# Optimization experiments

Measured on AMD Instinct MI355X. Metric: run time of the kernel, lower is better.

## Reference

```python
import jax, jax.numpy as jnp
import numpy as np

N_NODES = 100_000
N_EDGES = 1_600_000
IN_DIM = 64
OUT_DIM = 64
EPS = 1e-5


def setup_inputs() -> dict:
    key = jax.random.key(0)
    k1, k2, k3, k4, k5, k6 = jax.random.split(key, 6)
    node = jax.random.normal(k1, (N_NODES, 3), dtype=jnp.float32)
    features = jax.random.normal(k2, (N_NODES, IN_DIM), dtype=jnp.float32)
    # src column covers every node so torch.unique(edges[:,0]) == arange(N_NODES)
    src = (jnp.arange(N_EDGES, dtype=jnp.int64) % N_NODES)
    dst = jax.random.randint(k3, (N_EDGES,), 0, N_NODES, dtype=jnp.int64)
    edges = jnp.stack([src, dst], axis=1)
    # torch.nn.Linear weight: [out_dim, in_dim+3], no bias
    W = jax.random.normal(k4, (OUT_DIM, IN_DIM + 3), dtype=jnp.float32) / np.sqrt(IN_DIM + 3)
    gamma = jnp.ones((OUT_DIM,), dtype=jnp.float32)
    beta = jnp.zeros((OUT_DIM,), dtype=jnp.float32)
    return {"node": node, "features": features, "W": W, "gamma": gamma,
            "beta": beta, "edges": edges}


def reference(node, features, W, gamma, beta, edges):
    src = edges[:, 0]
    dst = edges[:, 1]
    # gather + concat: [E, in_dim + 3]
    msg = jnp.concatenate([features[dst], node[dst] - node[src]], axis=1)
    # linear (no bias): [E, out_dim]
    h = msg @ W.T
    # BatchNorm1d (training mode: biased batch statistics over E rows)
    mean = jnp.mean(h, axis=0)
    var = jnp.mean(jnp.square(h - mean), axis=0)
    h = (h - mean) * jax.lax.rsqrt(var + EPS) * gamma + beta
    h = jax.nn.relu(h)
    # scatter_reduce amax with include_self=True on a zeros tensor:
    # per-destination max, including the initial 0 (relu output >= 0 anyway)
    n = node.shape[0]
    pooled = jnp.zeros((n, h.shape[1]), dtype=features.dtype).at[src].max(h)
    return pooled
```

## Files before the change

kernel.cpp:

```cpp
#include <hip/hip_runtime.h>

#define N_NODES 100000
#define N_EDGES 1600000
#define EPS 1e-5f

typedef __bf16 bf16x8 __attribute__((ext_vector_type(8)));
typedef float  f32x4  __attribute__((ext_vector_type(4)));
typedef unsigned short u16x4 __attribute__((ext_vector_type(4)));

__device__ __forceinline__ unsigned short f2bf(float f) {
  return __builtin_bit_cast(unsigned short, static_cast<__bf16>(f));
}

__global__ __launch_bounds__(256) void prep_kernel(
    const float* __restrict__ feat, const float* __restrict__ W,
    unsigned short* __restrict__ featbf, unsigned short* __restrict__ Wbf) {
  int b = blockIdx.x, t = threadIdx.x;
  if (b < 6250) {
    int idx = (b * 256 + t) * 4;
    f32x4 v = *(const f32x4*)(feat + idx);
    u16x4 o;
    o[0] = f2bf(v[0]); o[1] = f2bf(v[1]); o[2] = f2bf(v[2]); o[3] = f2bf(v[3]);
    *(u16x4*)(featbf + idx) = o;
  } else {
    int wi = (b - 6250) * 256 + t;
    if (wi < 64 * 96) {
      int n = wi / 96, c = wi % 96;
      Wbf[wi] = (c < 67) ? f2bf(W[n * 67 + c]) : (unsigned short)0;
    }
  }
}

__global__ __launch_bounds__(256) void graph_kernel(
    const float* __restrict__ nodep, const int* __restrict__ edges,
    const unsigned short* __restrict__ featbf,
    const unsigned short* __restrict__ Wbf,
    float* __restrict__ maxv, float* __restrict__ minv,
    float* __restrict__ stats, int nwaves) {
  const int lane = threadIdx.x & 63;
  const int wave = (int)((blockIdx.x * blockDim.x + threadIdx.x) >> 6);
  const int c    = lane & 15;
  const int quad = lane >> 4;

  bf16x8 Bfrag[4][3];
#pragma unroll
  for (int t = 0; t < 4; ++t) {
    const unsigned short* wrow = Wbf + (t * 16 + c) * 96 + quad * 8;
#pragma unroll
    for (int s = 0; s < 3; ++s)
      Bfrag[t][s] = *(const bf16x8*)(wrow + s * 32);
  }

  float s1[4] = {0.f, 0.f, 0.f, 0.f};
  float s2[4] = {0.f, 0.f, 0.f, 0.f};

  for (int i = wave; i < N_NODES; i += nwaves) {
    int dst_own = 0;
    if (lane < 16) dst_own = edges[2 * (i + lane * N_NODES) + 1];
    int dst_m = __shfl(dst_own, c, 64);

    const unsigned short* frow = featbf + (size_t)dst_m * 64 + quad * 8;
    bf16x8 A0 = *(const bf16x8*)(frow);
    bf16x8 A1 = *(const bf16x8*)(frow + 32);

    bf16x8 A2;
#pragma unroll
    for (int j = 0; j < 8; ++j) A2[j] = (__bf16)0.0f;
    float nx = nodep[3 * i], ny = nodep[3 * i + 1], nz = nodep[3 * i + 2];
    if (quad == 0) {
      const float* dp = nodep + (size_t)dst_m * 3;
      A2[0] = (__bf16)(dp[0] - nx);
      A2[1] = (__bf16)(dp[1] - ny);
      A2[2] = (__bf16)(dp[2] - nz);
    }

    float mxw = 0.f, mnw = 0.f;
#pragma unroll
    for (int t = 0; t < 4; ++t) {
      f32x4 acc = {0.f, 0.f, 0.f, 0.f};
      acc = __builtin_amdgcn_mfma_f32_16x16x32_bf16(A0, Bfrag[t][0], acc, 0, 0, 0);
      acc = __builtin_amdgcn_mfma_f32_16x16x32_bf16(A1, Bfrag[t][1], acc, 0, 0, 0);
      acc = __builtin_amdgcn_mfma_f32_16x16x32_bf16(A2, Bfrag[t][2], acc, 0, 0, 0);

      float a0 = acc[0], a1 = acc[1], a2 = acc[2], a3 = acc[3];
      s1[t] += (a0 + a1) + (a2 + a3);
      s2[t] += (a0 * a0 + a1 * a1) + (a2 * a2 + a3 * a3);

      float mx = fmaxf(fmaxf(a0, a1), fmaxf(a2, a3));
      float mn = fminf(fminf(a0, a1), fminf(a2, a3));
      mx = fmaxf(mx, __shfl_xor(mx, 16, 64));
      mx = fmaxf(mx, __shfl_xor(mx, 32, 64));
      mn = fminf(mn, __shfl_xor(mn, 16, 64));
      mn = fminf(mn, __shfl_xor(mn, 32, 64));
      if (t == quad) { mxw = mx; mnw = mn; }
    }
    maxv[i * 64 + lane] = mxw;
    minv[i * 64 + lane] = mnw;
  }

#pragma unroll
  for (int t = 0; t < 4; ++t) {
    s1[t] += __shfl_xor(s1[t], 16, 64);
    s1[t] += __shfl_xor(s1[t], 32, 64);
    s2[t] += __shfl_xor(s2[t], 16, 64);
    s2[t] += __shfl_xor(s2[t], 32, 64);
  }
  float s1w = quad == 0 ? s1[0] : quad == 1 ? s1[1] : quad == 2 ? s1[2] : s1[3];
  float s2w = quad == 0 ? s2[0] : quad == 1 ? s2[1] : quad == 2 ? s2[2] : s2[3];
  stats[(size_t)lane * nwaves + wave]        = s1w;
  stats[(size_t)(64 + lane) * nwaves + wave] = s2w;
}

__global__ __launch_bounds__(256) void stats_kernel(
    const float* __restrict__ stats, const float* __restrict__ gamma,
    const float* __restrict__ beta, float* __restrict__ ss, int nwaves) {
  int d = blockIdx.x;
  int t = threadIdx.x;
  const float* r1 = stats + (size_t)d * nwaves;
  const float* r2 = stats + (size_t)(64 + d) * nwaves;
  float a = 0.f, b = 0.f;
  for (int k = t; k < nwaves; k += 256) { a += r1[k]; b += r2[k]; }
  __shared__ float l1[256], l2[256];
  l1[t] = a; l2[t] = b;
  __syncthreads();
  for (int s = 128; s > 0; s >>= 1) {
    if (t < s) { l1[t] += l1[t + s]; l2[t] += l2[t + s]; }
    __syncthreads();
  }
  if (t == 0) {
    const float inv_ne = 1.0f / (float)N_EDGES;
    float mean = l1[0] * inv_ne;
    float var  = fmaxf(l2[0] * inv_ne - mean * mean, 0.f);
    float sc   = gamma[d] * rsqrtf(var + EPS);
    ss[d]      = sc;
    ss[64 + d] = beta[d] - mean * sc;
  }
}

__global__ __launch_bounds__(256) void finalize_kernel(
    const float* __restrict__ minv, const float* __restrict__ ss,
    float* out) {
  int idx = blockIdx.x * 256 + threadIdx.x;
  int d = idx & 63;
  float sc = ss[d], sh = ss[64 + d];
  float v = (sc >= 0.f) ? out[idx] : minv[idx];
  out[idx] = fmaxf(fmaf(v, sc, sh), 0.f);
}

extern "C" void kernel_launch(void* const* d_in, const int* in_sizes, int n_in,
                              void* d_out, int out_size, void* d_ws, size_t ws_size,
                              hipStream_t stream) {
  const float* nodep = (const float*)d_in[0];
  const float* feat  = (const float*)d_in[1];
  const float* W     = (const float*)d_in[2];
  const float* gamma = (const float*)d_in[3];
  const float* beta  = (const float*)d_in[4];
  const int*   edges = (const int*)d_in[5];

  char* ws = (char*)d_ws;
  unsigned short* Wbf    = (unsigned short*)ws;
  unsigned short* featbf = (unsigned short*)(ws + 12288);
  float* minv  = (float*)(ws + 12288 + 12800000);
  float* stats = (float*)(ws + 12288 + 12800000 + 25600000);
  float* ss    = (float*)(ws + 12288 + 12800000 + 25600000 + 4194304);
  float* maxv  = (float*)d_out;

  const int nwaves = 8192;

  prep_kernel<<<6250 + 24, 256, 0, stream>>>(feat, W, featbf, Wbf);
  graph_kernel<<<nwaves / 4, 256, 0, stream>>>(nodep, edges, featbf, Wbf,
                                               maxv, minv, stats, nwaves);
  stats_kernel<<<64, 256, 0, stream>>>(stats, gamma, beta, ss, nwaves);
  finalize_kernel<<<25000, 256, 0, stream>>>(minv, ss, maxv);
}
```

Measured before the change: 174.6 us.

## Software-pipeline gathers in graph kernel with fixed per-wave node schedule

The graph kernel now uses 12500 waves, each handling exactly 8 nodes. All destination indices are preloaded in two registers up front, and the feature and position gathers for the next node are double-buffered so they overlap with the current node's MFMAs. Per-wave statistics are first reduced across the block in shared memory, which shrinks the stats buffer and the work left for the stats kernel. The cost is higher register pressure from the double buffers and a hardcoded node count and iteration schedule.

```diff
diff --git a/kernel.cpp b/kernel.cpp
--- a/kernel.cpp
+++ b/kernel.cpp
@@ -3,6 +3,10 @@
 #define N_NODES 100000
 #define N_EDGES 1600000
 #define EPS 1e-5f
+
+#define NW    12500
+#define ITERS 8
+#define NBLK  3125
 
 typedef __bf16 bf16x8 __attribute__((ext_vector_type(8)));
 typedef float  f32x4  __attribute__((ext_vector_type(4)));
@@ -36,7 +40,7 @@
     const unsigned short* __restrict__ featbf,
     const unsigned short* __restrict__ Wbf,
     float* __restrict__ maxv, float* __restrict__ minv,
-    float* __restrict__ stats, int nwaves) {
+    float* __restrict__ stats) {
   const int lane = threadIdx.x & 63;
   const int wave = (int)((blockIdx.x * blockDim.x + threadIdx.x) >> 6);
   const int c    = lane & 15;
@@ -51,36 +55,57 @@
       Bfrag[t][s] = *(const bf16x8*)(wrow + s * 32);
   }
 
+  int dstreg[2];
+  dstreg[0] = edges[2 * (wave + quad * NW + c * N_NODES) + 1];
+  dstreg[1] = edges[2 * (wave + (4 + quad) * NW + c * N_NODES) + 1];
+
   float s1[4] = {0.f, 0.f, 0.f, 0.f};
   float s2[4] = {0.f, 0.f, 0.f, 0.f};
 
-  for (int i = wave; i < N_NODES; i += nwaves) {
-    int dst_own = 0;
-    if (lane < 16) dst_own = edges[2 * (i + lane * N_NODES) + 1];
-    int dst_m = __shfl(dst_own, c, 64);
-
-    const unsigned short* frow = featbf + (size_t)dst_m * 64 + quad * 8;
-    bf16x8 A0 = *(const bf16x8*)(frow);
-    bf16x8 A1 = *(const bf16x8*)(frow + 32);
-
-    bf16x8 A2;
-#pragma unroll
-    for (int j = 0; j < 8; ++j) A2[j] = (__bf16)0.0f;
-    float nx = nodep[3 * i], ny = nodep[3 * i + 1], nz = nodep[3 * i + 2];
+  bf16x8 A0[2], A1[2];
+  float dpx[2], dpy[2], dpz[2];
+  float ox[2], oy[2], oz[2];
+
+  bf16x8 A2;
+#pragma unroll
+  for (int j = 0; j < 8; ++j) A2[j] = (__bf16)0.0f;
+
+  auto issue = [&](int b, int j, int dst) {
+    const unsigned short* frow = featbf + (size_t)dst * 64 + quad * 8;
+    A0[b] = *(const bf16x8*)(frow);
+    A1[b] = *(const bf16x8*)(frow + 32);
+    const float* dp = nodep + (size_t)dst * 3;
+    dpx[b] = dp[0]; dpy[b] = dp[1]; dpz[b] = dp[2];
+    int i = wave + j * NW;
+    ox[b] = nodep[3 * i]; oy[b] = nodep[3 * i + 1]; oz[b] = nodep[3 * i + 2];
+  };
+
+  int dst_cur = __shfl(dstreg[0], c, 64);
+  issue(0, 0, dst_cur);
+
+#pragma unroll
+  for (int j = 0; j < ITERS; ++j) {
+    const int b = j & 1;
+    if (j + 1 < ITERS) {
+      const int jn = j + 1;
+      int dst_next = __shfl(dstreg[jn >> 2], (jn & 3) * 16 + c, 64);
+      issue(b ^ 1, jn, dst_next);
+    }
+
     if (quad == 0) {
-      const float* dp = nodep + (size_t)dst_m * 3;
-      A2[0] = (__bf16)(dp[0] - nx);
-      A2[1] = (__bf16)(dp[1] - ny);
-      A2[2] = (__bf16)(dp[2] - nz);
-    }
-
+      A2[0] = (__bf16)(dpx[b] - ox[b]);
+      A2[1] = (__bf16)(dpy[b] - oy[b]);
+      A2[2] = (__bf16)(dpz[b] - oz[b]);
+    }
+
+    const int i = wave + j * NW;
     float mxw = 0.f, mnw = 0.f;
 #pragma unroll
     for (int t = 0; t < 4; ++t) {
       f32x4 acc = {0.f, 0.f, 0.f, 0.f};
-      acc = __builtin_amdgcn_mfma_f32_16x16x32_bf16(A0, Bfrag[t][0], acc, 0, 0, 0);
-      acc = __builtin_amdgcn_mfma_f32_16x16x32_bf16(A1, Bfrag[t][1], acc, 0, 0, 0);
-      acc = __builtin_amdgcn_mfma_f32_16x16x32_bf16(A2, Bfrag[t][2], acc, 0, 0, 0);
+      acc = __builtin_amdgcn_mfma_f32_16x16x32_bf16(A0[b], Bfrag[t][0], acc, 0, 0, 0);
+      acc = __builtin_amdgcn_mfma_f32_16x16x32_bf16(A1[b], Bfrag[t][1], acc, 0, 0, 0);
+      acc = __builtin_amdgcn_mfma_f32_16x16x32_bf16(A2,    Bfrag[t][2], acc, 0, 0, 0);
 
       float a0 = acc[0], a1 = acc[1], a2 = acc[2], a3 = acc[3];
       s1[t] += (a0 + a1) + (a2 + a3);
@@ -107,19 +132,32 @@
   }
   float s1w = quad == 0 ? s1[0] : quad == 1 ? s1[1] : quad == 2 ? s1[2] : s1[3];
   float s2w = quad == 0 ? s2[0] : quad == 1 ? s2[1] : quad == 2 ? s2[2] : s2[3];
-  stats[(size_t)lane * nwaves + wave]        = s1w;
-  stats[(size_t)(64 + lane) * nwaves + wave] = s2w;
+
+  __shared__ float redA[4][64], redB[4][64];
+  const int wv = threadIdx.x >> 6;
+  redA[wv][lane] = s1w;
+  redB[wv][lane] = s2w;
+  __syncthreads();
+  const int t = threadIdx.x;
+  if (t < 64) {
+    float a = (redA[0][t] + redA[1][t]) + (redA[2][t] + redA[3][t]);
+    stats[t * NBLK + blockIdx.x] = a;
+  } else if (t < 128) {
+    int d = t - 64;
+    float bsum = (redB[0][d] + redB[1][d]) + (redB[2][d] + redB[3][d]);
+    stats[(64 + d) * NBLK + blockIdx.x] = bsum;
+  }
 }
 
 __global__ __launch_bounds__(256) void stats_kernel(
     const float* __restrict__ stats, const float* __restrict__ gamma,
-    const float* __restrict__ beta, float* __restrict__ ss, int nwaves) {
+    const float* __restrict__ beta, float* __restrict__ ss) {
   int d = blockIdx.x;
   int t = threadIdx.x;
-  const float* r1 = stats + (size_t)d * nwaves;
-  const float* r2 = stats + (size_t)(64 + d) * nwaves;
+  const float* r1 = stats + (size_t)d * NBLK;
+  const float* r2 = stats + (size_t)(64 + d) * NBLK;
   float a = 0.f, b = 0.f;
-  for (int k = t; k < nwaves; k += 256) { a += r1[k]; b += r2[k]; }
+  for (int k = t; k < NBLK; k += 256) { a += r1[k]; b += r2[k]; }
   __shared__ float l1[256], l2[256];
   l1[t] = a; l2[t] = b;
   __syncthreads();
@@ -143,7 +181,8 @@
   int idx = blockIdx.x * 256 + threadIdx.x;
   int d = idx & 63;
   float sc = ss[d], sh = ss[64 + d];
-  float v = (sc >= 0.f) ? out[idx] : minv[idx];
+  float v = out[idx];
+  if (sc < 0.f) v = minv[idx];
   out[idx] = fmaxf(fmaf(v, sc, sh), 0.f);
 }
 
@@ -162,14 +201,12 @@
   unsigned short* featbf = (unsigned short*)(ws + 12288);
   float* minv  = (float*)(ws + 12288 + 12800000);
   float* stats = (float*)(ws + 12288 + 12800000 + 25600000);
-  float* ss    = (float*)(ws + 12288 + 12800000 + 25600000 + 4194304);
+  float* ss    = (float*)(ws + 12288 + 12800000 + 25600000 + 1600000);
   float* maxv  = (float*)d_out;
 
-  const int nwaves = 8192;
-
   prep_kernel<<<6250 + 24, 256, 0, stream>>>(feat, W, featbf, Wbf);
-  graph_kernel<<<nwaves / 4, 256, 0, stream>>>(nodep, edges, featbf, Wbf,
-                                               maxv, minv, stats, nwaves);
-  stats_kernel<<<64, 256, 0, stream>>>(stats, gamma, beta, ss, nwaves);
+  graph_kernel<<<NBLK, 256, 0, stream>>>(nodep, edges, featbf, Wbf,
+                                         maxv, minv, stats);
+  stats_kernel<<<64, 256, 0, stream>>>(stats, gamma, beta, ss);
   finalize_kernel<<<25000, 256, 0, stream>>>(minv, ss, maxv);
 }
```

After: 175.2 us. About the same (+0.4%).

## Select max or min by gamma sign in-kernel and restructure wave-to-node mapping

Applied to the files above, without the earlier changes.

Uses the sign of gamma to decide per channel whether the max or the min is needed, so only one value per node and channel is written. This drops the separate 25.6 MB min buffer and its read in finalize. The graph kernel now launches 25000 waves that each handle exactly 4 nodes, with all 64 edge indices loaded up front in one coalesced load. Per-wave statistics are pre-reduced through shared memory to per-block partials, which shrinks the stats buffer. The change relies on the sign of the BatchNorm scale depending only on gamma, which holds because rsqrt is positive.

```diff
diff --git a/kernel.cpp b/kernel.cpp
--- a/kernel.cpp
+++ b/kernel.cpp
@@ -3,6 +3,10 @@
 #define N_NODES 100000
 #define N_EDGES 1600000
 #define EPS 1e-5f
+
+#define NW    25000
+#define ITERS 4
+#define NBLK  6250
 
 typedef __bf16 bf16x8 __attribute__((ext_vector_type(8)));
 typedef float  f32x4  __attribute__((ext_vector_type(4)));
@@ -31,12 +35,12 @@
   }
 }
 
-__global__ __launch_bounds__(256) void graph_kernel(
+__global__ __launch_bounds__(256, 8) void graph_kernel(
     const float* __restrict__ nodep, const int* __restrict__ edges,
     const unsigned short* __restrict__ featbf,
     const unsigned short* __restrict__ Wbf,
-    float* __restrict__ maxv, float* __restrict__ minv,
-    float* __restrict__ stats, int nwaves) {
+    const float* __restrict__ gamma,
+    float* __restrict__ selv, float* __restrict__ stats) {
   const int lane = threadIdx.x & 63;
   const int wave = (int)((blockIdx.x * blockDim.x + threadIdx.x) >> 6);
   const int c    = lane & 15;
@@ -51,21 +55,26 @@
       Bfrag[t][s] = *(const bf16x8*)(wrow + s * 32);
   }
 
+  float gs = (gamma[lane] >= 0.f) ? 1.f : -1.f;
+
+  int dst_all = edges[2 * (wave + (lane >> 4) * NW + (lane & 15) * N_NODES) + 1];
+
   float s1[4] = {0.f, 0.f, 0.f, 0.f};
   float s2[4] = {0.f, 0.f, 0.f, 0.f};
 
-  for (int i = wave; i < N_NODES; i += nwaves) {
-    int dst_own = 0;
-    if (lane < 16) dst_own = edges[2 * (i + lane * N_NODES) + 1];
-    int dst_m = __shfl(dst_own, c, 64);
+  bf16x8 A2;
+#pragma unroll
+  for (int j = 0; j < 8; ++j) A2[j] = (__bf16)0.0f;
+
+#pragma unroll
+  for (int j = 0; j < ITERS; ++j) {
+    const int i = wave + j * NW;
+    int dst_m = __shfl(dst_all, j * 16 + c, 64);
 
     const unsigned short* frow = featbf + (size_t)dst_m * 64 + quad * 8;
     bf16x8 A0 = *(const bf16x8*)(frow);
     bf16x8 A1 = *(const bf16x8*)(frow + 32);
 
-    bf16x8 A2;
-#pragma unroll
-    for (int j = 0; j < 8; ++j) A2[j] = (__bf16)0.0f;
     float nx = nodep[3 * i], ny = nodep[3 * i + 1], nz = nodep[3 * i + 2];
     if (quad == 0) {
       const float* dp = nodep + (size_t)dst_m * 3;
@@ -74,7 +83,7 @@
       A2[2] = (__bf16)(dp[2] - nz);
     }
 
-    float mxw = 0.f, mnw = 0.f;
+    float selw = 0.f;
 #pragma unroll
     for (int t = 0; t < 4; ++t) {
       f32x4 acc = {0.f, 0.f, 0.f, 0.f};
@@ -86,16 +95,13 @@
       s1[t] += (a0 + a1) + (a2 + a3);
       s2[t] += (a0 * a0 + a1 * a1) + (a2 * a2 + a3 * a3);
 
-      float mx = fmaxf(fmaxf(a0, a1), fmaxf(a2, a3));
-      float mn = fminf(fminf(a0, a1), fminf(a2, a3));
+      float g = __shfl(gs, t * 16 + c, 64);
+      float mx = fmaxf(fmaxf(g * a0, g * a1), fmaxf(g * a2, g * a3));
       mx = fmaxf(mx, __shfl_xor(mx, 16, 64));
       mx = fmaxf(mx, __shfl_xor(mx, 32, 64));
-      mn = fminf(mn, __shfl_xor(mn, 16, 64));
-      mn = fminf(mn, __shfl_xor(mn, 32, 64));
-      if (t == quad) { mxw = mx; mnw = mn; }
+      if (t == quad) selw = g * mx;
     }
-    maxv[i * 64 + lane] = mxw;
-    minv[i * 64 + lane] = mnw;
+    selv[i * 64 + lane] = selw;
   }
 
 #pragma unroll
@@ -107,19 +113,32 @@
   }
   float s1w = quad == 0 ? s1[0] : quad == 1 ? s1[1] : quad == 2 ? s1[2] : s1[3];
   float s2w = quad == 0 ? s2[0] : quad == 1 ? s2[1] : quad == 2 ? s2[2] : s2[3];
-  stats[(size_t)lane * nwaves + wave]        = s1w;
-  stats[(size_t)(64 + lane) * nwaves + wave] = s2w;
+
+  __shared__ float redA[4][64], redB[4][64];
+  const int wv = threadIdx.x >> 6;
+  redA[wv][lane] = s1w;
+  redB[wv][lane] = s2w;
+  __syncthreads();
+  const int t = threadIdx.x;
+  if (t < 64) {
+    float a = (redA[0][t] + redA[1][t]) + (redA[2][t] + redA[3][t]);
+    stats[t * NBLK + blockIdx.x] = a;
+  } else if (t < 128) {
+    int d = t - 64;
+    float bsum = (redB[0][d] + redB[1][d]) + (redB[2][d] + redB[3][d]);
+    stats[(64 + d) * NBLK + blockIdx.x] = bsum;
+  }
 }
 
 __global__ __launch_bounds__(256) void stats_kernel(
     const float* __restrict__ stats, const float* __restrict__ gamma,
-    const float* __restrict__ beta, float* __restrict__ ss, int nwaves) {
+    const float* __restrict__ beta, float* __restrict__ ss) {
   int d = blockIdx.x;
   int t = threadIdx.x;
-  const float* r1 = stats + (size_t)d * nwaves;
-  const float* r2 = stats + (size_t)(64 + d) * nwaves;
+  const float* r1 = stats + (size_t)d * NBLK;
+  const float* r2 = stats + (size_t)(64 + d) * NBLK;
   float a = 0.f, b = 0.f;
-  for (int k = t; k < nwaves; k += 256) { a += r1[k]; b += r2[k]; }
+  for (int k = t; k < NBLK; k += 256) { a += r1[k]; b += r2[k]; }
   __shared__ float l1[256], l2[256];
   l1[t] = a; l2[t] = b;
   __syncthreads();
@@ -138,13 +157,10 @@
 }
 
 __global__ __launch_bounds__(256) void finalize_kernel(
-    const float* __restrict__ minv, const float* __restrict__ ss,
-    float* out) {
+    const float* __restrict__ ss, float* out) {
   int idx = blockIdx.x * 256 + threadIdx.x;
   int d = idx & 63;
-  float sc = ss[d], sh = ss[64 + d];
-  float v = (sc >= 0.f) ? out[idx] : minv[idx];
-  out[idx] = fmaxf(fmaf(v, sc, sh), 0.f);
+  out[idx] = fmaxf(fmaf(out[idx], ss[d], ss[64 + d]), 0.f);
 }
 
 extern "C" void kernel_launch(void* const* d_in, const int* in_sizes, int n_in,
@@ -160,16 +176,13 @@
   char* ws = (char*)d_ws;
   unsigned short* Wbf    = (unsigned short*)ws;
   unsigned short* featbf = (unsigned short*)(ws + 12288);
-  float* minv  = (float*)(ws + 12288 + 12800000);
-  float* stats = (float*)(ws + 12288 + 12800000 + 25600000);
-  float* ss    = (float*)(ws + 12288 + 12800000 + 25600000 + 4194304);
-  float* maxv  = (float*)d_out;
-
-  const int nwaves = 8192;
+  float* stats = (float*)(ws + 12288 + 12800000);
+  float* ss    = (float*)(ws + 12288 + 12800000 + 3200000);
+  float* selv  = (float*)d_out;
 
   prep_kernel<<<6250 + 24, 256, 0, stream>>>(feat, W, featbf, Wbf);
-  graph_kernel<<<nwaves / 4, 256, 0, stream>>>(nodep, edges, featbf, Wbf,
-                                               maxv, minv, stats, nwaves);
-  stats_kernel<<<64, 256, 0, stream>>>(stats, gamma, beta, ss, nwaves);
-  finalize_kernel<<<25000, 256, 0, stream>>>(minv, ss, maxv);
+  graph_kernel<<<NBLK, 256, 0, stream>>>(nodep, edges, featbf, Wbf, gamma,
+                                         selv, stats);
+  stats_kernel<<<64, 256, 0, stream>>>(stats, gamma, beta, ss);
+  finalize_kernel<<<25000, 256, 0, stream>>>(ss, selv);
 }
```

New measurement: 406.8 us. +133.0%, slower.
